# Kernel tuning notes

Hardware: AMD Instinct MI355X
Metric: run time of the kernel (lower is better)

Reference implementation:

```python
import jax, jax.numpy as jnp
import numpy as np

RADIUS = 0.2
NSAMPLE = 32
EPS = 1e-5  # BatchNorm2d default eps


def _bn_relu(x, g, b):
    # BatchNorm2d in training mode: per-channel stats over (B, S, nsample), biased var.
    m = x.mean(axis=(0, 1, 2))
    v = jnp.mean((x - m) ** 2, axis=(0, 1, 2))
    return jax.nn.relu((x - m) * jax.lax.rsqrt(v + EPS) * g + b)


def setup_inputs() -> dict:
    key = jax.random.key(0)
    ks = jax.random.split(key, 8)
    B, N, S = 8, 8192, 2048
    xyz = jax.random.uniform(ks[0], (B, 3, N), dtype=jnp.float32)          # unit cube
    points = jax.random.normal(ks[1], (B, 3, N), dtype=jnp.float32)
    fps_idx = jax.random.randint(ks[2], (B, S), 0, N, dtype=jnp.int32)
    W1 = jax.random.normal(ks[3], (64, 6), dtype=jnp.float32) * 0.1
    W2 = jax.random.normal(ks[4], (64, 64), dtype=jnp.float32) * 0.1
    W3 = jax.random.normal(ks[5], (128, 64), dtype=jnp.float32) * 0.1
    return dict(
        xyz=xyz, points=points, fps_idx=fps_idx,
        W1=W1, g1=jnp.ones((64,)), b1=jnp.zeros((64,)),
        W2=W2, g2=jnp.ones((64,)), b2=jnp.zeros((64,)),
        W3=W3, g3=jnp.ones((128,)), b3=jnp.zeros((128,)),
    )


def reference(xyz, points, fps_idx, W1, g1, b1, W2, g2, b2, W3, g3, b3):
    B, _, N = xyz.shape
    xyz_t = jnp.transpose(xyz, (0, 2, 1))            # [B,N,3]
    pts_t = jnp.transpose(points, (0, 2, 1))         # [B,N,D]
    # gather_operation: sampled centers
    new_xyz_t = jnp.take_along_axis(xyz_t, fps_idx[:, :, None], axis=1)  # [B,S,3]
    # ball query: first NSAMPLE points within radius; pad with first hit
    d2 = jnp.sum((new_xyz_t[:, :, None, :] - xyz_t[:, None, :, :]) ** 2, axis=-1)  # [B,S,N]
    keys = jnp.where(d2 <= RADIUS * RADIUS, jnp.arange(N, dtype=jnp.int32), N)
    neg_top, _ = jax.lax.top_k(-keys, NSAMPLE)       # smallest keys first
    idx = -neg_top                                   # [B,S,NSAMPLE]
    idx = jnp.where(idx < N, idx, idx[:, :, 0:1])    # pad empty slots with first hit (self always in-radius)
    bidx = jnp.arange(B)[:, None, None]
    grouped_xyz = xyz_t[bidx, idx]                   # [B,S,ns,3]
    rel = grouped_xyz - new_xyz_t[:, :, None, :]     # center-relative coords
    grouped_pts = pts_t[bidx, idx]                   # [B,S,ns,D]
    feat = jnp.concatenate([rel, grouped_pts], axis=-1)  # [B,S,ns,3+D]
    for W, g, b in ((W1, g1, b1), (W2, g2, b2), (W3, g3, b3)):
        feat = _bn_relu(jnp.einsum('bsnc,oc->bsno', feat, W), g, b)
    new_points = jnp.max(feat, axis=2)               # max over neighbors -> [B,S,C]
    return jnp.transpose(new_xyz_t, (0, 2, 1)), jnp.transpose(new_points, (0, 2, 1))
```

## Files before the change

kernel.cpp:

```cpp
#include <hip/hip_runtime.h>
#include <hip/hip_bf16.h>

#define BB_ 8
#define NN_ 8192
#define SS_ 2048
#define NS 32
#define C1 64
#define C2 64
#define C3 128
#define RAD2 0.04f
#define BN_EPS 1e-5f
#define M_TOT (BB_*SS_*NS)
#define INV_M (1.0f/524288.0f)
#define YSTR 34

typedef __attribute__((ext_vector_type(8))) short bf16x8;
typedef __attribute__((ext_vector_type(4))) float f32x4;

#define FBF_OFF 0
#define WPK_OFF 2097152
#define ST_OFF  2104320
#define GMM_OFF 2104832
#define X2_OFF  4201984
#define WS_NEED ((size_t)(4201984 + 16777216) * 4)

__device__ inline unsigned pkbf(float a, float b) {
    __hip_bfloat162 h = __float22bfloat162_rn(make_float2(a, b));
    unsigned r; __builtin_memcpy(&r, &h, 4); return r;
}
__device__ inline bf16x8 asfrag(uint4 v) { bf16x8 r; __builtin_memcpy(&r, &v, 16); return r; }
__device__ inline float bflo(unsigned u) { unsigned x = u << 16; float f; __builtin_memcpy(&f, &x, 4); return f; }
__device__ inline float bfhi(unsigned u) { unsigned x = u & 0xffff0000u; float f; __builtin_memcpy(&f, &x, 4); return f; }

__device__ inline void fin1_ch(const float* __restrict__ st, const float* __restrict__ W1,
                               const float* __restrict__ g, const float* __restrict__ bb,
                               int o, float* __restrict__ al, float* __restrict__ cl) {
    float w[6];
    #pragma unroll
    for (int i = 0; i < 6; ++i) w[i] = W1[o * 6 + i];
    float ms = 0.f;
    #pragma unroll
    for (int i = 0; i < 6; ++i) ms = fmaf(w[i], st[i], ms);
    float m = ms * INV_M;
    float e2 = 0.f;
    #pragma unroll
    for (int ci = 0; ci < 6; ++ci)
        #pragma unroll
        for (int d = 0; d < 6; ++d) {
            int lo = ci < d ? ci : d, hi = ci < d ? d : ci;
            int idx = 6 + lo * 6 - lo * (lo + 1) / 2 + hi;
            e2 = fmaf(w[ci] * w[d], st[idx], e2);
        }
    float var = e2 * INV_M - m * m;
    float ai = g[o] * (1.0f / sqrtf(var + BN_EPS));
    al[o] = ai;
    cl[o] = bb[o] - m * ai;
}

__device__ inline void fin_ch(const float* __restrict__ sum, const float* __restrict__ sq,
                              const float* __restrict__ g, const float* __restrict__ bb,
                              int o, float* __restrict__ al, float* __restrict__ cl) {
    float m = sum[o] * INV_M;
    float var = sq[o] * INV_M - m * m;
    float ai = g[o] * (1.0f / sqrtf(var + BN_EPS));
    al[o] = ai;
    cl[o] = bb[o] - m * ai;
}

__global__ void k_front(const float* __restrict__ xyz, const float* __restrict__ pts,
                        const int* __restrict__ fps, uint4* __restrict__ fbf,
                        const float* __restrict__ W1, const float* __restrict__ W2,
                        const float* __restrict__ W3, uint4* __restrict__ wf,
                        float* __restrict__ st) {
    __shared__ int lidx[4][NS];
    int tid = threadIdx.x;
    if (blockIdx.x >= 4096) {
        int bb = blockIdx.x - 4096;
        if (bb == 7) { st[tid] = 0.f; st[tid + 256] = 0.f; return; }
        int t = bb * 256 + tid;
        int l = t & 63, p = l & 15, qd = l >> 4;
        float v[8];
        if (t < 256) {
            int mt = t >> 6;
            #pragma unroll
            for (int j = 0; j < 8; ++j)
                v[j] = (qd == 0 && j < 6) ? W1[(mt * 16 + p) * 6 + j] : 0.f;
        } else if (t < 768) {
            int fr = (t - 256) >> 6;
            int mt = fr >> 1, kf = fr & 1;
            #pragma unroll
            for (int j = 0; j < 8; ++j)
                v[j] = W2[(16 * mt + p) * 64 + kf * 32 + qd * 8 + j];
        } else {
            int fr = (t - 768) >> 6;
            int nt = fr >> 1, kf = fr & 1;
            #pragma unroll
            for (int j = 0; j < 8; ++j)
                v[j] = W3[(nt * 16 + p) * 64 + kf * 32 + qd * 8 + j];
        }
        uint4 o;
        o.x = pkbf(v[0], v[1]); o.y = pkbf(v[2], v[3]);
        o.z = pkbf(v[4], v[5]); o.w = pkbf(v[6], v[7]);
        wf[t] = o;
        return;
    }
    int wave = (blockIdx.x * blockDim.x + tid) >> 6;
    int lane = tid & 63;
    int wslot = tid >> 6;
    int b = wave / SS_;
    const float* xb = xyz + (size_t)b * 3 * NN_;
    const float* pb = pts + (size_t)b * 3 * NN_;
    int ci = fps[wave];
    float cx = xb[ci], cy = xb[NN_ + ci], cz = xb[2 * NN_ + ci];

    float px = xb[lane], py = xb[NN_ + lane], pz = xb[2 * NN_ + lane];
    int found = 0;
    int first_i = -1;
    for (int base = 0; base < NN_; base += 64) {
        float xv = px, yv = py, zv = pz;
        int nb = (base + 64 < NN_) ? base + 64 : 0;
        px = xb[nb + lane]; py = xb[NN_ + nb + lane]; pz = xb[2 * NN_ + nb + lane];
        float dx = xv - cx, dy = yv - cy, dz = zv - cz;
        float d2 = __fadd_rn(__fadd_rn(__fmul_rn(dx, dx), __fmul_rn(dy, dy)), __fmul_rn(dz, dz));
        bool inr = d2 <= RAD2;
        unsigned long long mask = __ballot(inr);
        if (first_i < 0 && mask) first_i = base + __builtin_ctzll(mask);
        if (inr) {
            int pos = found + __popcll(mask & ((1ull << lane) - 1ull));
            if (pos < NS) lidx[wslot][pos] = base + lane;
        }
        found += __popcll(mask);
        if (found >= NS) break;
    }
    if (found > NS) found = NS;
    if (lane < NS) {
        int j = (lane < found) ? lidx[wslot][lane] : first_i;
        uint4 o;
        o.x = pkbf(xb[j] - cx,           xb[NN_ + j] - cy);
        o.y = pkbf(xb[2 * NN_ + j] - cz, pb[j]);
        o.z = pkbf(pb[NN_ + j],          pb[2 * NN_ + j]);
        o.w = 0u;
        fbf[(size_t)wave * NS + lane] = o;
    }
}

__global__ void k_p1(const uint4* __restrict__ fbf, float* __restrict__ st) {
    __shared__ float sacc[27];
    int tid = threadIdx.x;
    if (tid < 27) sacc[tid] = 0.f;
    __syncthreads();
    int gt = blockIdx.x * 256 + tid;
    float vals[27];
    #pragma unroll
    for (int i = 0; i < 27; ++i) vals[i] = 0.f;
    #pragma unroll 1
    for (int it = 0; it < M_TOT / 65536; ++it) {
        uint4 w = fbf[it * 65536 + gt];
        float f[6] = { bflo(w.x), bfhi(w.x), bflo(w.y), bfhi(w.y), bflo(w.z), bfhi(w.z) };
        #pragma unroll
        for (int c = 0; c < 6; ++c) vals[c] += f[c];
        int q = 6;
        #pragma unroll
        for (int c = 0; c < 6; ++c)
            #pragma unroll
            for (int d = c; d < 6; ++d) { vals[q] = fmaf(f[c], f[d], vals[q]); ++q; }
    }
    int lane = tid & 63;
    #pragma unroll
    for (int i = 0; i < 27; ++i) {
        float v = vals[i];
        #pragma unroll
        for (int d = 32; d; d >>= 1) v += __shfl_xor(v, d);
        if (lane == 0) atomicAdd(&sacc[i], v);
    }
    __syncthreads();
    if (tid < 27) atomicAdd(&st[tid], sacc[tid]);
}

__global__ __launch_bounds__(128) void k_p2(
        const uint4* __restrict__ fbf, const uint4* __restrict__ wpk,
        float* __restrict__ st,
        const float* __restrict__ W1, const float* __restrict__ g1, const float* __restrict__ b1,
        uint4* __restrict__ x2a, int store_x2) {
    __shared__ unsigned yls[2][64 * YSTR];
    __shared__ float bs[C2], bq[C2];
    __shared__ float a1ls[C1], c1ls[C1];
    int tid = threadIdx.x, wslot = tid >> 6, lane = tid & 63;
    int p = lane & 15, qd = lane >> 4;
    if (tid < C2) { bs[tid] = 0.f; bq[tid] = 0.f; fin1_ch(st, W1, g1, b1, tid, a1ls, c1ls); }
    __syncthreads();
    const uint4* w1f = wpk;
    const uint4* w2f = wpk + 256;
    unsigned* my = yls[wslot];
    float s2[4][4], q2[4][4];
    #pragma unroll
    for (int i = 0; i < 4; ++i)
        #pragma unroll
        for (int r = 0; r < 4; ++r) { s2[i][r] = 0.f; q2[i][r] = 0.f; }

    #pragma unroll 1
    for (int it = 0; it < 4; ++it) {
        int tile = it * 2048 + blockIdx.x * 2 + wslot;
        int base = tile * 64;
        bf16x8 B1[4];
        #pragma unroll
        for (int nt = 0; nt < 4; ++nt) {
            uint4 v = make_uint4(0u, 0u, 0u, 0u);
            if (qd == 0) v = fbf[base + nt * 16 + p];
            B1[nt] = asfrag(v);
        }
        #pragma unroll
        for (int mt = 0; mt < 4; ++mt) {
            bf16x8 A = asfrag(w1f[mt * 64 + lane]);
            float4 av = *(const float4*)(a1ls + mt * 16 + qd * 4);
            float4 cv = *(const float4*)(c1ls + mt * 16 + qd * 4);
            #pragma unroll
            for (int nt = 0; nt < 4; ++nt) {
                f32x4 acc = {0.f, 0.f, 0.f, 0.f};
                acc = __builtin_amdgcn_mfma_f32_16x16x32_bf16(A, B1[nt], acc, 0, 0, 0);
                float y0 = fmaxf(fmaf(av.x, acc[0], cv.x), 0.f);
                float y1 = fmaxf(fmaf(av.y, acc[1], cv.y), 0.f);
                float y2 = fmaxf(fmaf(av.z, acc[2], cv.z), 0.f);
                float y3 = fmaxf(fmaf(av.w, acc[3], cv.w), 0.f);
                int a = (nt * 16 + p) * YSTR + mt * 8 + qd * 2;
                *(uint2*)&my[a] = make_uint2(pkbf(y0, y1), pkbf(y2, y3));
            }
        }
        __syncthreads();
        bf16x8 B2[4][2];
        #pragma unroll
        for (int nt = 0; nt < 4; ++nt)
            #pragma unroll
            for (int kf = 0; kf < 2; ++kf)
                B2[nt][kf] = asfrag(*(const uint4*)&my[(nt * 16 + p) * YSTR + kf * 16 + qd * 4]);
        __syncthreads();
        #pragma unroll
        for (int mt = 0; mt < 4; ++mt) {
            f32x4 acc[4];
            #pragma unroll
            for (int nt = 0; nt < 4; ++nt) acc[nt] = (f32x4){0.f, 0.f, 0.f, 0.f};
            #pragma unroll
            for (int kf = 0; kf < 2; ++kf) {
                bf16x8 W = asfrag(w2f[(mt * 2 + kf) * 64 + lane]);
                #pragma unroll
                for (int nt = 0; nt < 4; ++nt)
                    acc[nt] = __builtin_amdgcn_mfma_f32_16x16x32_bf16(W, B2[nt][kf], acc[nt], 0, 0, 0);
            }
            if (store_x2) {
                #pragma unroll
                for (int nt = 0; nt < 4; ++nt) {
                    int a = (nt * 16 + p) * YSTR + mt * 8 + qd * 2;
                    *(uint2*)&my[a] = make_uint2(pkbf(acc[nt][0], acc[nt][1]),
                                                 pkbf(acc[nt][2], acc[nt][3]));
                }
            }
            #pragma unroll
            for (int r = 0; r < 4; ++r) {
                float u0 = acc[0][r], u1 = acc[1][r], u2 = acc[2][r], u3 = acc[3][r];
                s2[mt][r] += (u0 + u1) + (u2 + u3);
                q2[mt][r] = fmaf(u0, u0, fmaf(u1, u1, fmaf(u2, u2, fmaf(u3, u3, q2[mt][r]))));
            }
        }
        if (store_x2) {
            __syncthreads();
            #pragma unroll
            for (int mtc = 0; mtc < 4; ++mtc)
                #pragma unroll
                for (int kf = 0; kf < 2; ++kf) {
                    uint4 v = *(const uint4*)&my[(mtc * 16 + p) * YSTR + kf * 16 + qd * 4];
                    x2a[((size_t)tile * 8 + mtc * 2 + kf) * 64 + lane] = v;
                }
        }
        __syncthreads();
    }
    #pragma unroll
    for (int mt = 0; mt < 4; ++mt)
        #pragma unroll
        for (int r = 0; r < 4; ++r) {
            float s = s2[mt][r], q = q2[mt][r];
            #pragma unroll
            for (int off = 1; off <= 8; off <<= 1) { s += __shfl_xor(s, off); q += __shfl_xor(q, off); }
            if (p == 0) {
                atomicAdd(&bs[mt * 16 + qd * 4 + r], s);
                atomicAdd(&bq[mt * 16 + qd * 4 + r], q);
            }
        }
    __syncthreads();
    if (tid < C2) { atomicAdd(&st[64 + tid], bs[tid]); atomicAdd(&st[128 + tid], bq[tid]); }
}

__global__ __launch_bounds__(256) void k_p3_l3(
        const uint4* __restrict__ x2a, const uint4* __restrict__ wpk,
        float* __restrict__ st,
        const float* __restrict__ g2, const float* __restrict__ b2,
        const float* __restrict__ g3, float* __restrict__ gmm) {
    __shared__ uint4 w3ls[1024];
    __shared__ float bs[C3], bq[C3];
    __shared__ float a2ls[C2], c2ls[C2];
    int tid = threadIdx.x, wslot = tid >> 6, lane = tid & 63;
    int p = lane & 15, qd = lane >> 4;
    if (tid < 128) bs[tid] = 0.f; else bq[tid - 128] = 0.f;
    #pragma unroll
    for (int i = 0; i < 4; ++i) w3ls[i * 256 + tid] = wpk[768 + i * 256 + tid];
    if (tid < C2) fin_ch(st + 64, st + 128, g2, b2, tid, a2ls, c2ls);
    __syncthreads();
    float a2r[2][8], c2r[2][8];
    #pragma unroll
    for (int kf = 0; kf < 2; ++kf)
        #pragma unroll
        for (int j = 0; j < 8; ++j) {
            a2r[kf][j] = a2ls[kf * 32 + qd * 8 + j];
            c2r[kf][j] = c2ls[kf * 32 + qd * 8 + j];
        }
    float gs3[8], gq3[8], va[8], vb[8];
    bool pos[8];
    #pragma unroll
    for (int i = 0; i < 8; ++i) {
        gs3[i] = 0.f; gq3[i] = 0.f; va[i] = -3.4e38f; vb[i] = -3.4e38f;
        pos[i] = g3[i * 16 + p] >= 0.f;
    }
    int tile = blockIdx.x * 4 + wslot;
    size_t cb = (size_t)tile * 8;

    uint4 c0 = x2a[(cb + 0) * 64 + lane];
    uint4 c1 = x2a[(cb + 1) * 64 + lane];
    #pragma unroll 1
    for (int mt = 0; mt < 4; ++mt) {
        uint4 n0 = c0, n1 = c1;
        if (mt < 3) {
            n0 = x2a[(cb + (mt + 1) * 2 + 0) * 64 + lane];
            n1 = x2a[(cb + (mt + 1) * 2 + 1) * 64 + lane];
        }
        bf16x8 A0, A1;
        {
            unsigned w0[4] = { c0.x, c0.y, c0.z, c0.w };
            unsigned w1[4] = { c1.x, c1.y, c1.z, c1.w };
            unsigned r0[4], r1[4];
            #pragma unroll
            for (int wi = 0; wi < 4; ++wi) {
                float lo0 = bflo(w0[wi]), hi0 = bfhi(w0[wi]);
                r0[wi] = pkbf(fmaxf(fmaf(a2r[0][2 * wi], lo0, c2r[0][2 * wi]), 0.f),
                              fmaxf(fmaf(a2r[0][2 * wi + 1], hi0, c2r[0][2 * wi + 1]), 0.f));
                float lo1 = bflo(w1[wi]), hi1 = bfhi(w1[wi]);
                r1[wi] = pkbf(fmaxf(fmaf(a2r[1][2 * wi], lo1, c2r[1][2 * wi]), 0.f),
                              fmaxf(fmaf(a2r[1][2 * wi + 1], hi1, c2r[1][2 * wi + 1]), 0.f));
            }
            uint4 t0 = make_uint4(r0[0], r0[1], r0[2], r0[3]);
            uint4 t1 = make_uint4(r1[0], r1[1], r1[2], r1[3]);
            A0 = asfrag(t0); A1 = asfrag(t1);
        }
        int g = mt >> 1;
        #pragma unroll
        for (int nt = 0; nt < 8; ++nt) {
            bf16x8 Wa = asfrag(w3ls[(nt * 2 + 0) * 64 + lane]);
            bf16x8 Wb = asfrag(w3ls[(nt * 2 + 1) * 64 + lane]);
            f32x4 acc = __builtin_amdgcn_mfma_f32_16x16x32_bf16(A0, Wa,
                            (f32x4){0.f, 0.f, 0.f, 0.f}, 0, 0, 0);
            acc = __builtin_amdgcn_mfma_f32_16x16x32_bf16(A1, Wb, acc, 0, 0, 0);
            float v0 = acc[0], v1 = acc[1], v2 = acc[2], v3 = acc[3];
            gs3[nt] += (v0 + v1) + (v2 + v3);
            gq3[nt] = fmaf(v0, v0, fmaf(v1, v1, fmaf(v2, v2, fmaf(v3, v3, gq3[nt]))));
            float mx = fmaxf(fmaxf(v0, v1), fmaxf(v2, v3));
            float mn = fminf(fminf(v0, v1), fminf(v2, v3));
            float vv = pos[nt] ? mx : -mn;
            if (g == 0) va[nt] = fmaxf(va[nt], vv);
            else        vb[nt] = fmaxf(vb[nt], vv);
        }
        c0 = n0; c1 = n1;
    }
    #pragma unroll
    for (int nt = 0; nt < 8; ++nt) {
        float x = va[nt], y = vb[nt];
        x = fmaxf(x, __shfl_xor(x, 16)); x = fmaxf(x, __shfl_xor(x, 32));
        y = fmaxf(y, __shfl_xor(y, 16)); y = fmaxf(y, __shfl_xor(y, 32));
        if (lane < 16) {
            gmm[(size_t)(tile * 2 + 0) * C3 + nt * 16 + lane] = x;
            gmm[(size_t)(tile * 2 + 1) * C3 + nt * 16 + lane] = y;
        }
    }
    #pragma unroll
    for (int nt = 0; nt < 8; ++nt) {
        float s = gs3[nt], q = gq3[nt];
        s += __shfl_xor(s, 16); s += __shfl_xor(s, 32);
        q += __shfl_xor(q, 16); q += __shfl_xor(q, 32);
        if (lane < 16) {
            atomicAdd(&bs[nt * 16 + lane], s);
            atomicAdd(&bq[nt * 16 + lane], q);
        }
    }
    __syncthreads();
    if (tid < C3) { atomicAdd(&st[192 + tid], bs[tid]); atomicAdd(&st[320 + tid], bq[tid]); }
}

__global__ __launch_bounds__(256) void k_p3_fused(
        const uint4* __restrict__ fbf, const uint4* __restrict__ wpk,
        float* __restrict__ st,
        const float* __restrict__ W1, const float* __restrict__ g1, const float* __restrict__ b1,
        const float* __restrict__ g2, const float* __restrict__ b2,
        const float* __restrict__ g3, float* __restrict__ gmm) {
    __shared__ unsigned yls[4][64 * YSTR];
    __shared__ uint4 w3ls[1024];
    __shared__ float bs[C3], bq[C3];
    __shared__ float a1ls[C1], c1ls[C1], a2ls[C2], c2ls[C2];
    int tid = threadIdx.x, wslot = tid >> 6, lane = tid & 63;
    int p = lane & 15, qd = lane >> 4;
    if (tid < 128) bs[tid] = 0.f; else bq[tid - 128] = 0.f;
    #pragma unroll
    for (int i = 0; i < 4; ++i) w3ls[i * 256 + tid] = wpk[768 + i * 256 + tid];
    if (tid < 64) fin1_ch(st, W1, g1, b1, tid, a1ls, c1ls);
    else if (tid < 128) fin_ch(st + 64, st + 128, g2, b2, tid - 64, a2ls, c2ls);
    __syncthreads();
    const uint4* w1f = wpk;
    const uint4* w2f = wpk + 256;
    unsigned* my = yls[wslot];
    float gs3[8], gq3[8];
    bool pos[8];
    #pragma unroll
    for (int i = 0; i < 8; ++i) { gs3[i] = 0.f; gq3[i] = 0.f; pos[i] = g3[i * 16 + p] >= 0.f; }

    #pragma unroll 1
    for (int it = 0; it < 2; ++it) {
        int tile = it * 4096 + blockIdx.x * 4 + wslot;
        int base = tile * 64;
        bf16x8 B1[4];
        #pragma unroll
        for (int nt = 0; nt < 4; ++nt) {
            uint4 v = make_uint4(0u, 0u, 0u, 0u);
            if (qd == 0) v = fbf[base + nt * 16 + p];
            B1[nt] = asfrag(v);
        }
        #pragma unroll
        for (int mt = 0; mt < 4; ++mt) {
            bf16x8 A = asfrag(w1f[mt * 64 + lane]);
            float4 av = *(const float4*)(a1ls + mt * 16 + qd * 4);
            float4 cv = *(const float4*)(c1ls + mt * 16 + qd * 4);
            #pragma unroll
            for (int nt = 0; nt < 4; ++nt) {
                f32x4 acc = {0.f, 0.f, 0.f, 0.f};
                acc = __builtin_amdgcn_mfma_f32_16x16x32_bf16(A, B1[nt], acc, 0, 0, 0);
                float y0 = fmaxf(fmaf(av.x, acc[0], cv.x), 0.f);
                float y1 = fmaxf(fmaf(av.y, acc[1], cv.y), 0.f);
                float y2 = fmaxf(fmaf(av.z, acc[2], cv.z), 0.f);
                float y3 = fmaxf(fmaf(av.w, acc[3], cv.w), 0.f);
                int a = (nt * 16 + p) * YSTR + mt * 8 + qd * 2;
                *(uint2*)&my[a] = make_uint2(pkbf(y0, y1), pkbf(y2, y3));
            }
        }
        __syncthreads();
        bf16x8 B2[4][2];
        #pragma unroll
        for (int nt = 0; nt < 4; ++nt)
            #pragma unroll
            for (int kf = 0; kf < 2; ++kf)
                B2[nt][kf] = asfrag(*(const uint4*)&my[(nt * 16 + p) * YSTR + kf * 16 + qd * 4]);
        __syncthreads();
        #pragma unroll
        for (int mt = 0; mt < 4; ++mt) {
            f32x4 acc[4];
            #pragma unroll
            for (int nt = 0; nt < 4; ++nt) acc[nt] = (f32x4){0.f, 0.f, 0.f, 0.f};
            #pragma unroll
            for (int kf = 0; kf < 2; ++kf) {
                bf16x8 W = asfrag(w2f[(mt * 2 + kf) * 64 + lane]);
                #pragma unroll
                for (int nt = 0; nt < 4; ++nt)
                    acc[nt] = __builtin_amdgcn_mfma_f32_16x16x32_bf16(W, B2[nt][kf], acc[nt], 0, 0, 0);
            }
            float4 av = *(const float4*)(a2ls + mt * 16 + qd * 4);
            float4 cv = *(const float4*)(c2ls + mt * 16 + qd * 4);
            #pragma unroll
            for (int nt = 0; nt < 4; ++nt) {
                float y0 = fmaxf(fmaf(av.x, acc[nt][0], cv.x), 0.f);
                float y1 = fmaxf(fmaf(av.y, acc[nt][1], cv.y), 0.f);
                float y2 = fmaxf(fmaf(av.z, acc[nt][2], cv.z), 0.f);
                float y3 = fmaxf(fmaf(av.w, acc[nt][3], cv.w), 0.f);
                int a = (nt * 16 + p) * YSTR + mt * 8 + qd * 2;
                *(uint2*)&my[a] = make_uint2(pkbf(y0, y1), pkbf(y2, y3));
            }
        }
        __syncthreads();
        bf16x8 A3[4][2];
        #pragma unroll
        for (int mt = 0; mt < 4; ++mt) {
            A3[mt][0] = asfrag(*(const uint4*)&my[(mt * 16 + p) * YSTR + qd * 4]);
            A3[mt][1] = asfrag(*(const uint4*)&my[(mt * 16 + p) * YSTR + 16 + qd * 4]);
        }
        __syncthreads();
        #pragma unroll
        for (int nt = 0; nt < 8; ++nt) {
            bf16x8 Wa = asfrag(w3ls[(nt * 2 + 0) * 64 + lane]);
            bf16x8 Wb = asfrag(w3ls[(nt * 2 + 1) * 64 + lane]);
            f32x4 acc[4];
            #pragma unroll
            for (int mt = 0; mt < 4; ++mt) {
                acc[mt] = __builtin_amdgcn_mfma_f32_16x16x32_bf16(A3[mt][0], Wa,
                            (f32x4){0.f, 0.f, 0.f, 0.f}, 0, 0, 0);
                acc[mt] = __builtin_amdgcn_mfma_f32_16x16x32_bf16(A3[mt][1], Wb, acc[mt], 0, 0, 0);
            }
            float s = 0.f, q = 0.f, va = 0.f, vb = 0.f;
            #pragma unroll
            for (int mt = 0; mt < 4; ++mt) {
                float v0 = acc[mt][0], v1 = acc[mt][1], v2 = acc[mt][2], v3 = acc[mt][3];
                s += (v0 + v1) + (v2 + v3);
                q = fmaf(v0, v0, fmaf(v1, v1, fmaf(v2, v2, fmaf(v3, v3, q))));
                float mx = fmaxf(fmaxf(v0, v1), fmaxf(v2, v3));
                float mn = fminf(fminf(v0, v1), fminf(v2, v3));
                float vv = pos[nt] ? mx : -mn;
                if (mt == 0) va = vv;
                else if (mt == 1) va = fmaxf(va, vv);
                else if (mt == 2) vb = vv;
                else vb = fmaxf(vb, vv);
            }
            gs3[nt] += s; gq3[nt] += q;
            va = fmaxf(va, __shfl_xor(va, 16)); va = fmaxf(va, __shfl_xor(va, 32));
            vb = fmaxf(vb, __shfl_xor(vb, 16)); vb = fmaxf(vb, __shfl_xor(vb, 32));
            if (lane < 16) {
                gmm[(size_t)(tile * 2 + 0) * C3 + nt * 16 + lane] = va;
                gmm[(size_t)(tile * 2 + 1) * C3 + nt * 16 + lane] = vb;
            }
        }
    }
    #pragma unroll
    for (int nt = 0; nt < 8; ++nt) {
        float s = gs3[nt], q = gq3[nt];
        s += __shfl_xor(s, 16); s += __shfl_xor(s, 32);
        q += __shfl_xor(q, 16); q += __shfl_xor(q, 32);
        if (lane < 16) {
            atomicAdd(&bs[nt * 16 + lane], s);
            atomicAdd(&bq[nt * 16 + lane], q);
        }
    }
    __syncthreads();
    if (tid < C3) { atomicAdd(&st[192 + tid], bs[tid]); atomicAdd(&st[320 + tid], bq[tid]); }
}

__global__ void k_outx(const float* __restrict__ gmm, const float* __restrict__ st,
                       const float* __restrict__ g3, const float* __restrict__ b3,
                       const float* __restrict__ xyz, const int* __restrict__ fps,
                       float* __restrict__ out) {
    __shared__ float T[C3][17];
    __shared__ float a3ls[C3], c3ls[C3];
    int blk = blockIdx.x, tid = threadIdx.x;
    if (blk < 1024) {
        if (tid < C3) fin_ch(st + 192, st + 320, g3, b3, tid, a3ls, c3ls);
        __syncthreads();
        int b = blk >> 7, s0 = (blk & 127) << 4;
        #pragma unroll
        for (int i = 0; i < 8; ++i) {
            int idx = i * 256 + tid;
            int sl = idx >> 7, o = idx & 127;
            float m = gmm[((size_t)(b * SS_ + s0 + sl)) * C3 + o];
            float a = a3ls[o];
            float v = (a >= 0.f) ? m : -m;
            T[o][sl] = fmaxf(fmaf(a, v, c3ls[o]), 0.f);
        }
        __syncthreads();
        int o = tid & 127, sh = tid >> 7;
        float* dst = out + (size_t)BB_ * 3 * SS_ + ((size_t)b * C3 + o) * SS_ + s0 + sh * 8;
        float4 w0, w1;
        w0.x = T[o][sh * 8 + 0]; w0.y = T[o][sh * 8 + 1];
        w0.z = T[o][sh * 8 + 2]; w0.w = T[o][sh * 8 + 3];
        w1.x = T[o][sh * 8 + 4]; w1.y = T[o][sh * 8 + 5];
        w1.z = T[o][sh * 8 + 6]; w1.w = T[o][sh * 8 + 7];
        *(float4*)dst = w0; *(float4*)(dst + 4) = w1;
    } else {
        int t = (blk - 1024) * 256 + tid;
        int b = t / (3 * SS_);
        int r = (t / SS_) % 3;
        int s = t % SS_;
        int ci = fps[b * SS_ + s];
        out[t] = xyz[((size_t)b * 3 + r) * NN_ + ci];
    }
}

extern "C" void kernel_launch(void* const* d_in, const int* in_sizes, int n_in,
                              void* d_out, int out_size, void* d_ws, size_t ws_size,
                              hipStream_t stream) {
    (void)in_sizes; (void)n_in; (void)out_size;
    const float* xyz = (const float*)d_in[0];
    const float* pts = (const float*)d_in[1];
    const int*   fps = (const int*)d_in[2];
    const float* W1 = (const float*)d_in[3];
    const float* g1 = (const float*)d_in[4];
    const float* b1 = (const float*)d_in[5];
    const float* W2 = (const float*)d_in[6];
    const float* g2 = (const float*)d_in[7];
    const float* b2 = (const float*)d_in[8];
    const float* W3 = (const float*)d_in[9];
    const float* g3 = (const float*)d_in[10];
    const float* b3 = (const float*)d_in[11];
    float* out = (float*)d_out;
    float* ws = (float*)d_ws;

    uint4* fbf = (uint4*)(ws + FBF_OFF);
    uint4* wpk = (uint4*)(ws + WPK_OFF);
    float* st  = ws + ST_OFF;
    float* gmm = ws + GMM_OFF;
    uint4* x2a = (uint4*)(ws + X2_OFF);
    int split = (ws_size >= WS_NEED) ? 1 : 0;

    k_front<<<4096 + 8, 256, 0, stream>>>(xyz, pts, fps, fbf, W1, W2, W3, wpk, st);
    k_p1<<<256, 256, 0, stream>>>(fbf, st);
    k_p2<<<1024, 128, 0, stream>>>(fbf, wpk, st, W1, g1, b1, x2a, split);
    if (split)
        k_p3_l3<<<2048, 256, 0, stream>>>(x2a, wpk, st, g2, b2, g3, gmm);
    else
        k_p3_fused<<<1024, 256, 0, stream>>>(fbf, wpk, st, W1, g1, b1, g2, b2, g3, gmm);
    k_outx<<<1024 + 192, 256, 0, stream>>>(gmm, st, g3, b3, xyz, fps, out);
}
```

Measured before the change: 247.5 us.

## Process four tiles per wave in layer-3 kernel with whole-tile prefetch

```diff
diff --git a/kernel.cpp b/kernel.cpp
--- a/kernel.cpp
+++ b/kernel.cpp
@@ -312,70 +312,76 @@
             a2r[kf][j] = a2ls[kf * 32 + qd * 8 + j];
             c2r[kf][j] = c2ls[kf * 32 + qd * 8 + j];
         }
-    float gs3[8], gq3[8], va[8], vb[8];
+    float gs3[8], gq3[8];
     bool pos[8];
     #pragma unroll
-    for (int i = 0; i < 8; ++i) {
-        gs3[i] = 0.f; gq3[i] = 0.f; va[i] = -3.4e38f; vb[i] = -3.4e38f;
-        pos[i] = g3[i * 16 + p] >= 0.f;
-    }
-    int tile = blockIdx.x * 4 + wslot;
-    size_t cb = (size_t)tile * 8;
-
-    uint4 c0 = x2a[(cb + 0) * 64 + lane];
-    uint4 c1 = x2a[(cb + 1) * 64 + lane];
+    for (int i = 0; i < 8; ++i) { gs3[i] = 0.f; gq3[i] = 0.f; pos[i] = g3[i * 16 + p] >= 0.f; }
+
+    int wv = blockIdx.x * 4 + wslot;
+    size_t cb = (size_t)wv * 4 * 8;
+
+    uint4 cur[8], nxt[8];
+    #pragma unroll
+    for (int i = 0; i < 8; ++i) cur[i] = x2a[(cb + i) * 64 + lane];
+
     #pragma unroll 1
-    for (int mt = 0; mt < 4; ++mt) {
-        uint4 n0 = c0, n1 = c1;
-        if (mt < 3) {
-            n0 = x2a[(cb + (mt + 1) * 2 + 0) * 64 + lane];
-            n1 = x2a[(cb + (mt + 1) * 2 + 1) * 64 + lane];
-        }
-        bf16x8 A0, A1;
-        {
-            unsigned w0[4] = { c0.x, c0.y, c0.z, c0.w };
-            unsigned w1[4] = { c1.x, c1.y, c1.z, c1.w };
-            unsigned r0[4], r1[4];
-            #pragma unroll
-            for (int wi = 0; wi < 4; ++wi) {
-                float lo0 = bflo(w0[wi]), hi0 = bfhi(w0[wi]);
-                r0[wi] = pkbf(fmaxf(fmaf(a2r[0][2 * wi], lo0, c2r[0][2 * wi]), 0.f),
-                              fmaxf(fmaf(a2r[0][2 * wi + 1], hi0, c2r[0][2 * wi + 1]), 0.f));
-                float lo1 = bflo(w1[wi]), hi1 = bfhi(w1[wi]);
-                r1[wi] = pkbf(fmaxf(fmaf(a2r[1][2 * wi], lo1, c2r[1][2 * wi]), 0.f),
-                              fmaxf(fmaf(a2r[1][2 * wi + 1], hi1, c2r[1][2 * wi + 1]), 0.f));
-            }
-            uint4 t0 = make_uint4(r0[0], r0[1], r0[2], r0[3]);
-            uint4 t1 = make_uint4(r1[0], r1[1], r1[2], r1[3]);
-            A0 = asfrag(t0); A1 = asfrag(t1);
-        }
-        int g = mt >> 1;
+    for (int t = 0; t < 4; ++t) {
+        int tile = wv * 4 + t;
+        if (t < 3) {
+            #pragma unroll
+            for (int i = 0; i < 8; ++i) nxt[i] = x2a[(cb + (t + 1) * 8 + i) * 64 + lane];
+        }
+        bf16x8 A[4][2];
+        #pragma unroll
+        for (int mt = 0; mt < 4; ++mt)
+            #pragma unroll
+            for (int kf = 0; kf < 2; ++kf) {
+                uint4 u = cur[mt * 2 + kf];
+                unsigned w[4] = { u.x, u.y, u.z, u.w };
+                unsigned r[4];
+                #pragma unroll
+                for (int wi = 0; wi < 4; ++wi) {
+                    float lo = bflo(w[wi]), hi = bfhi(w[wi]);
+                    r[wi] = pkbf(fmaxf(fmaf(a2r[kf][2 * wi], lo, c2r[kf][2 * wi]), 0.f),
+                                 fmaxf(fmaf(a2r[kf][2 * wi + 1], hi, c2r[kf][2 * wi + 1]), 0.f));
+                }
+                uint4 o = make_uint4(r[0], r[1], r[2], r[3]);
+                A[mt][kf] = asfrag(o);
+            }
+        float va[2][8];
         #pragma unroll
         for (int nt = 0; nt < 8; ++nt) {
             bf16x8 Wa = asfrag(w3ls[(nt * 2 + 0) * 64 + lane]);
             bf16x8 Wb = asfrag(w3ls[(nt * 2 + 1) * 64 + lane]);
-            f32x4 acc = __builtin_amdgcn_mfma_f32_16x16x32_bf16(A0, Wa,
-                            (f32x4){0.f, 0.f, 0.f, 0.f}, 0, 0, 0);
-            acc = __builtin_amdgcn_mfma_f32_16x16x32_bf16(A1, Wb, acc, 0, 0, 0);
-            float v0 = acc[0], v1 = acc[1], v2 = acc[2], v3 = acc[3];
-            gs3[nt] += (v0 + v1) + (v2 + v3);
-            gq3[nt] = fmaf(v0, v0, fmaf(v1, v1, fmaf(v2, v2, fmaf(v3, v3, gq3[nt]))));
-            float mx = fmaxf(fmaxf(v0, v1), fmaxf(v2, v3));
-            float mn = fminf(fminf(v0, v1), fminf(v2, v3));
-            float vv = pos[nt] ? mx : -mn;
-            if (g == 0) va[nt] = fmaxf(va[nt], vv);
-            else        vb[nt] = fmaxf(vb[nt], vv);
-        }
-        c0 = n0; c1 = n1;
-    }
-    #pragma unroll
-    for (int nt = 0; nt < 8; ++nt) {
-        float x = va[nt], y = vb[nt];
-        x = fmaxf(x, __shfl_xor(x, 16)); x = fmaxf(x, __shfl_xor(x, 32));
-        y = fmaxf(y, __shfl_xor(y, 16)); y = fmaxf(y, __shfl_xor(y, 32));
-        if (lane < 16) {
-            gmm[(size_t)(tile * 2 + 0) * C3 + nt * 16 + lane] = x;
-            gmm[(size_t)(tile * 2 + 1) * C3 + nt * 16 + lane] = y;
+            #pragma unroll
+            for (int mt = 0; mt < 4; ++mt) {
+                f32x4 acc = __builtin_amdgcn_mfma_f32_16x16x32_bf16(A[mt][0], Wa,
+                                (f32x4){0.f, 0.f, 0.f, 0.f}, 0, 0, 0);
+                acc = __builtin_amdgcn_mfma_f32_16x16x32_bf16(A[mt][1], Wb, acc, 0, 0, 0);
+                float v0 = acc[0], v1 = acc[1], v2 = acc[2], v3 = acc[3];
+                gs3[nt] += (v0 + v1) + (v2 + v3);
+                gq3[nt] = fmaf(v0, v0, fmaf(v1, v1, fmaf(v2, v2, fmaf(v3, v3, gq3[nt]))));
+                float mx = fmaxf(fmaxf(v0, v1), fmaxf(v2, v3));
+                float mn = fminf(fminf(v0, v1), fminf(v2, v3));
+                float vv = pos[nt] ? mx : -mn;
+                int g = mt >> 1;
+                if ((mt & 1) == 0) va[g][nt] = vv;
+                else va[g][nt] = fmaxf(va[g][nt], vv);
+            }
+        }
+        #pragma unroll
+        for (int nt = 0; nt < 8; ++nt) {
+            float x = va[0][nt], y = va[1][nt];
+            x = fmaxf(x, __shfl_xor(x, 16)); x = fmaxf(x, __shfl_xor(x, 32));
+            y = fmaxf(y, __shfl_xor(y, 16)); y = fmaxf(y, __shfl_xor(y, 32));
+            if (lane < 16) {
+                gmm[(size_t)(tile * 2 + 0) * C3 + nt * 16 + lane] = x;
+                gmm[(size_t)(tile * 2 + 1) * C3 + nt * 16 + lane] = y;
+            }
+        }
+        if (t < 3) {
+            #pragma unroll
+            for (int i = 0; i < 8; ++i) cur[i] = nxt[i];
         }
     }
     #pragma unroll
@@ -431,13 +437,13 @@
         }
         #pragma unroll
         for (int mt = 0; mt < 4; ++mt) {
-            bf16x8 A = asfrag(w1f[mt * 64 + lane]);
+            bf16x8 Aw = asfrag(w1f[mt * 64 + lane]);
             float4 av = *(const float4*)(a1ls + mt * 16 + qd * 4);
             float4 cv = *(const float4*)(c1ls + mt * 16 + qd * 4);
             #pragma unroll
             for (int nt = 0; nt < 4; ++nt) {
                 f32x4 acc = {0.f, 0.f, 0.f, 0.f};
-                acc = __builtin_amdgcn_mfma_f32_16x16x32_bf16(A, B1[nt], acc, 0, 0, 0);
+                acc = __builtin_amdgcn_mfma_f32_16x16x32_bf16(Aw, B1[nt], acc, 0, 0, 0);
                 float y0 = fmaxf(fmaf(av.x, acc[0], cv.x), 0.f);
                 float y1 = fmaxf(fmaf(av.y, acc[1], cv.y), 0.f);
                 float y2 = fmaxf(fmaf(av.z, acc[2], cv.z), 0.f);
@@ -603,7 +609,7 @@
     k_p1<<<256, 256, 0, stream>>>(fbf, st);
     k_p2<<<1024, 128, 0, stream>>>(fbf, wpk, st, W1, g1, b1, x2a, split);
     if (split)
-        k_p3_l3<<<2048, 256, 0, stream>>>(x2a, wpk, st, g2, b2, g3, gmm);
+        k_p3_l3<<<512, 256, 0, stream>>>(x2a, wpk, st, g2, b2, g3, gmm);
     else
         k_p3_fused<<<1024, 256, 0, stream>>>(fbf, wpk, st, W1, g1, b1, g2, b2, g3, gmm);
     k_outx<<<1024 + 192, 256, 0, stream>>>(gmm, st, g3, b3, xyz, fps, out);
```

Result: faster. 226.0 us (-8.7%).
